# Kernel optimization log

Measured on AMD Instinct MI355X. Metric: run time of the kernel, lower is better.

Reference implementation:

```python
import jax, jax.numpy as jnp
import numpy as np

HEADS = 64
VOCAB = 5
EPS = 1e-5

def _layer_norm(x, g, b):
    mu = jnp.mean(x, axis=-1, keepdims=True)
    var = jnp.var(x, axis=-1, keepdims=True)
    return (x - mu) * jax.lax.rsqrt(var + EPS) * g + b

def setup_inputs() -> dict:
    key = jax.random.key(0)
    ks = jax.random.split(key, 12)
    h = HEADS
    s = 1.0 / np.sqrt(h)
    return {
        "x": jax.random.normal(ks[0], (8, 384, 384, h), dtype=jnp.float32),
        "W1": jax.random.normal(ks[1], (h, h), dtype=jnp.float32) * s,
        "b1": jnp.zeros((h,), jnp.float32),
        "W2": jax.random.normal(ks[2], (h, h), dtype=jnp.float32) * s,
        "b2": jnp.zeros((h,), jnp.float32),
        "W3": jax.random.normal(ks[3], (h, h), dtype=jnp.float32) * s,
        "b3": jnp.zeros((h,), jnp.float32),
        "ln_g": jnp.ones((h,), jnp.float32),
        "ln_b": jnp.zeros((h,), jnp.float32),
        "Wo": jax.random.normal(ks[4], (h, VOCAB), dtype=jnp.float32) * s,
        "bo": jnp.zeros((VOCAB,), jnp.float32),
    }

def reference(x, W1, b1, W2, b2, W3, b3, ln_g, ln_b, Wo, bo):
    # three (Linear -> gelu -> shared LayerNorm) blocks on [b,s,s,h]
    h = _layer_norm(jax.nn.gelu(x @ W1 + b1, approximate=False), ln_g, ln_b)
    h = _layer_norm(jax.nn.gelu(h @ W2 + b2, approximate=False), ln_g, ln_b)
    h = _layer_norm(jax.nn.gelu(h @ W3 + b3, approximate=False), ln_g, ln_b)
    out = h @ Wo + bo  # [b,s,s,vocab]
    return (out + jnp.swapaxes(out, 1, 2)) * 0.5
```

## Files before the change

kernel.cpp:

```cpp
#include <hip/hip_runtime.h>
#include <cstdint>
#include <cstddef>

typedef __attribute__((ext_vector_type(8))) __bf16   bf16x8;
typedef __attribute__((ext_vector_type(2))) __bf16   bf16x2;
typedef __attribute__((ext_vector_type(4))) float    f32x4;
typedef __attribute__((ext_vector_type(4))) uint32_t u32x4;

#define N_ROWS   1179648
#define N_TILES  73728
#define BLOCKS   2048
#define TPW      9
#define SDIM     384
#define VOCAB    5

#define WO_OFF   24576
#define BIAS_OFF 26624
#define OUT_OFF  27392

__device__ __forceinline__ f32x4 gelu4(f32x4 x){
  f32x4 u = x * x;
  f32x4 w = u * (-0.10294456f) + (-2.3021255f);
  f32x4 z = x * w;
  f32x4 e;
  e[0] = __builtin_amdgcn_exp2f(z[0]);
  e[1] = __builtin_amdgcn_exp2f(z[1]);
  e[2] = __builtin_amdgcn_exp2f(z[2]);
  e[3] = __builtin_amdgcn_exp2f(z[3]);
  f32x4 d = e + 1.0f;
  f32x4 r;
  r[0] = __builtin_amdgcn_rcpf(d[0]);
  r[1] = __builtin_amdgcn_rcpf(d[1]);
  r[2] = __builtin_amdgcn_rcpf(d[2]);
  r[3] = __builtin_amdgcn_rcpf(d[3]);
  return x * r;
}

__device__ __forceinline__ bf16x8 mk_bf8(f32x4 a, f32x4 b){
  bf16x8 v;
  v[0]=(__bf16)a[0]; v[1]=(__bf16)a[1]; v[2]=(__bf16)a[2]; v[3]=(__bf16)a[3];
  v[4]=(__bf16)b[0]; v[5]=(__bf16)b[1]; v[6]=(__bf16)b[2]; v[7]=(__bf16)b[3];
  return v;
}

__device__ __forceinline__ int perm_rho(int m){
  return (m & 0x23) | ((m & 4) << 2) | ((m & 0x18) >> 1);
}

__global__ __launch_bounds__(256, 4)
void mlp_kernel(const float* __restrict__ x,
                const float* __restrict__ W1, const float* __restrict__ b1,
                const float* __restrict__ W2, const float* __restrict__ b2,
                const float* __restrict__ W3, const float* __restrict__ b3,
                const float* __restrict__ lng, const float* __restrict__ lnb,
                const float* __restrict__ Wo,  const float* __restrict__ bo,
                float* __restrict__ tmp)
{
  __shared__ __align__(16) uint8_t Wl[28672];

  const int tid = threadIdx.x;

  {
    int m = tid & 63, g = tid >> 6;
    int rho = perm_rho(m);
    uint8_t* wrow = Wl + rho * 128;
    int swz = (rho & 7) << 4;
    #pragma unroll 1
    for (int idx = g; idx < 96; idx += 4) {
      int L = idx >> 5, kp = idx & 31;
      const float* W = (L == 0) ? W1 : ((L == 1) ? W2 : W3);
      float g0 = (L == 0) ? 1.0f : lng[2 * kp];
      float g1 = (L == 0) ? 1.0f : lng[2 * kp + 1];
      float lo = W[(2 * kp    ) * 64 + m] * g0;
      float hi = W[(2 * kp + 1) * 64 + m] * g1;
      bf16x2 p = { (__bf16)lo, (__bf16)hi };
      *(uint32_t*)(wrow + L * 8192 + ((4 * kp) ^ swz)) = __builtin_bit_cast(uint32_t, p);
    }
    int mm = tid & 15;
    #pragma unroll 1
    for (int kp = tid >> 4; kp < 32; kp += 16) {
      float g0 = lng[2 * kp], g1 = lng[2 * kp + 1];
      float lo = (mm < VOCAB) ? Wo[(2 * kp    ) * VOCAB + mm] * g0 : 0.0f;
      float hi = (mm < VOCAB) ? Wo[(2 * kp + 1) * VOCAB + mm] * g1 : 0.0f;
      bf16x2 p = { (__bf16)lo, (__bf16)hi };
      *(uint32_t*)(Wl + WO_OFF + mm * 128 + ((4 * kp) ^ ((mm & 7) << 4))) =
          __builtin_bit_cast(uint32_t, p);
    }
    if (tid < 128) {
      int m2 = tid & 63;
      const float* W = (tid < 64) ? W2 : W3;
      float d = (tid < 64) ? b2[m2] : b3[m2];
      #pragma unroll 4
      for (int k = 0; k < 64; ++k) d = __builtin_fmaf(W[k * 64 + m2], lnb[k], d);
      *(float*)(Wl + BIAS_OFF + (64 + tid) * 4) = d;
    } else if (tid < 192) {
      *(float*)(Wl + BIAS_OFF + (tid - 128) * 4) = b1[tid - 128];
    }
  }
  __syncthreads();

  const int wav  = tid >> 6, lane = tid & 63;
  const int h    = lane >> 4;
  const int b    = lane & 15;
  const int swzW = (b & 7) << 4;
  const int rowB = b * 128;
  const int kOff = 16 * h;
  const float* biasL = (const float*)(Wl + BIAS_OFF);
  float* myF = (float*)(Wl + OUT_OFF) + wav * 80;

  f32x4 aoInit;
  #pragma unroll
  for (int r = 0; r < 4; ++r) {
    int v = 4 * h + r;
    aoInit[r] = (v < VOCAB) ? bo[v] : 0.0f;
  }
  #pragma unroll 4
  for (int k = 0; k < 64; ++k) {
    float l = lnb[k];
    #pragma unroll
    for (int r = 0; r < 4; ++r) {
      int v = 4 * h + r;
      if (v < VOCAB) aoInit[r] = __builtin_fmaf(l, Wo[k * VOCAB + v], aoInit[r]);
    }
  }

  const int gw = blockIdx.x * 4 + wav;
  int t = gw * TPW;

  f32x4 xn[4];
  {
    const float* px = x + (size_t)(t * 16 + b) * 64 + 8 * h;
    xn[0] = *(const f32x4*)(px);      xn[1] = *(const f32x4*)(px + 4);
    xn[2] = *(const f32x4*)(px + 32); xn[3] = *(const f32x4*)(px + 36);
  }

  #pragma unroll 1
  for (int i = 0; i < TPW; ++i, ++t) {
    u32x4 bfr[2];
    bfr[0] = __builtin_bit_cast(u32x4, mk_bf8(xn[0], xn[1]));
    bfr[1] = __builtin_bit_cast(u32x4, mk_bf8(xn[2], xn[3]));

    {
      int tn = (i + 1 < TPW) ? (t + 1) : t;
      const float* pn = x + (size_t)(tn * 16 + b) * 64 + 8 * h;
      xn[0] = *(const f32x4*)(pn);      xn[1] = *(const f32x4*)(pn + 4);
      xn[2] = *(const f32x4*)(pn + 32); xn[3] = *(const f32x4*)(pn + 36);
    }

    #pragma unroll
    for (int L = 0; L < 3; ++L) {
      const uint8_t* wp = Wl + L * 8192 + rowB;
      f32x4 acc[4];
      #pragma unroll
      for (int mt = 0; mt < 4; ++mt) {
        u32x4 w0 = *(const u32x4*)(wp + mt * 2048 + ((kOff     ) ^ swzW));
        u32x4 w1 = *(const u32x4*)(wp + mt * 2048 + ((kOff + 64) ^ swzW));
        int base = 8 * h + 4 * (mt & 1) + 32 * (mt >> 1);
        acc[mt] = *(const f32x4*)(biasL + L * 64 + base);
        acc[mt] = __builtin_amdgcn_mfma_f32_16x16x32_bf16(
            __builtin_bit_cast(bf16x8, w0), __builtin_bit_cast(bf16x8, bfr[0]), acc[mt], 0, 0, 0);
        acc[mt] = __builtin_amdgcn_mfma_f32_16x16x32_bf16(
            __builtin_bit_cast(bf16x8, w1), __builtin_bit_cast(bf16x8, bfr[1]), acc[mt], 0, 0, 0);
      }

      #pragma unroll
      for (int mt = 0; mt < 4; ++mt) acc[mt] = gelu4(acc[mt]);

      f32x4 vs = acc[0] + acc[1] + acc[2] + acc[3];
      f32x4 vq = acc[0]*acc[0] + acc[1]*acc[1] + acc[2]*acc[2] + acc[3]*acc[3];
      float s1 = (vs[0]+vs[1]) + (vs[2]+vs[3]);
      float s2 = (vq[0]+vq[1]) + (vq[2]+vq[3]);
      s1 += __shfl_xor(s1, 16); s2 += __shfl_xor(s2, 16);
      s1 += __shfl_xor(s1, 32); s2 += __shfl_xor(s2, 32);
      float mu   = s1 * (1.0f/64.0f);
      float var  = __builtin_fmaf(s2, (1.0f/64.0f), -mu * mu);
      float rstd = rsqrtf(var + 1e-5f);
      float nm   = -mu * rstd;

      f32x4 n0 = acc[0] * rstd + nm;
      f32x4 n1 = acc[1] * rstd + nm;
      f32x4 n2 = acc[2] * rstd + nm;
      f32x4 n3 = acc[3] * rstd + nm;
      bfr[0] = __builtin_bit_cast(u32x4, mk_bf8(n0, n1));
      bfr[1] = __builtin_bit_cast(u32x4, mk_bf8(n2, n3));
    }

    f32x4 ao = aoInit;
    {
      const uint8_t* wp = Wl + WO_OFF + rowB;
      u32x4 w0 = *(const u32x4*)(wp + ((kOff     ) ^ swzW));
      u32x4 w1 = *(const u32x4*)(wp + ((kOff + 64) ^ swzW));
      ao = __builtin_amdgcn_mfma_f32_16x16x32_bf16(
          __builtin_bit_cast(bf16x8, w0), __builtin_bit_cast(bf16x8, bfr[0]), ao, 0, 0, 0);
      ao = __builtin_amdgcn_mfma_f32_16x16x32_bf16(
          __builtin_bit_cast(bf16x8, w1), __builtin_bit_cast(bf16x8, bfr[1]), ao, 0, 0, 0);
    }

    #pragma unroll
    for (int r = 0; r < 4; ++r) {
      int v = 4 * h + r;
      if (v < VOCAB) myF[b * VOCAB + v] = ao[r];
    }
    float* dst = tmp + (size_t)t * 80;
    dst[lane] = myF[lane];
    if (lane < 16) dst[64 + lane] = myF[64 + lane];
  }
}

__global__ __launch_bounds__(256)
void sym_kernel(const float* __restrict__ tmp, float* __restrict__ out)
{
  __shared__ float A[32][164];
  __shared__ float B[32][164];
  int bid = blockIdx.x;
  int bb = bid / 144, r2 = bid - bb * 144;
  int ti = r2 / 12,  tj = r2 - ti * 12;
  int i0 = ti * 32,  j0 = tj * 32;
  const size_t base = (size_t)bb * SDIM * SDIM;

  for (int idx = threadIdx.x; idx < 32 * 160; idx += 256) {
    int r = idx / 160, c = idx - r * 160;
    A[r][c] = tmp[(base + (size_t)(i0 + r) * SDIM + j0) * VOCAB + c];
    B[r][c] = tmp[(base + (size_t)(j0 + r) * SDIM + i0) * VOCAB + c];
  }
  __syncthreads();
  for (int idx = threadIdx.x; idx < 32 * 160; idx += 256) {
    int r = idx / 160, c = idx - r * 160;
    int jc = c / 5, v = c - jc * 5;
    out[(base + (size_t)(i0 + r) * SDIM + j0) * VOCAB + c] =
        0.5f * (A[r][c] + B[jc][r * 5 + v]);
  }
}

extern "C" void kernel_launch(void* const* d_in, const int* in_sizes, int n_in,
                              void* d_out, int out_size, void* d_ws, size_t ws_size,
                              hipStream_t stream)
{
  const float* x   = (const float*)d_in[0];
  const float* W1  = (const float*)d_in[1];
  const float* b1  = (const float*)d_in[2];
  const float* W2  = (const float*)d_in[3];
  const float* b2  = (const float*)d_in[4];
  const float* W3  = (const float*)d_in[5];
  const float* b3  = (const float*)d_in[6];
  const float* lng = (const float*)d_in[7];
  const float* lnb = (const float*)d_in[8];
  const float* Wo  = (const float*)d_in[9];
  const float* bo  = (const float*)d_in[10];

  float* tmp = (float*)d_ws;
  float* out = (float*)d_out;

  mlp_kernel<<<BLOCKS, 256, 0, stream>>>(x, W1, b1, W2, b2, W3, b3,
                                         lng, lnb, Wo, bo, tmp);
  sym_kernel<<<8 * 12 * 12, 256, 0, stream>>>(tmp, out);
}
```

Baseline: 167.8 us.

## Fold LayerNorm normalization into following matmul epilogue via precomputed weight sums

Instead of normalizing the activations before each bf16 pack, the kernel packs the raw gelu outputs and applies rstd and the mean correction after the next MFMA. It uses precomputed per-column sums of gamma-scaled weights, stored in extra LDS. This removes the per-element normalize step before packing and moves the work to the accumulator epilogue. It also drops the occupancy hint from launch bounds. Numerics change because unnormalized values are rounded to bf16, which risks precision loss for large-magnitude activations.

```diff
diff --git a/kernel.cpp b/kernel.cpp
--- a/kernel.cpp
+++ b/kernel.cpp
@@ -16,7 +16,7 @@
 
 #define WO_OFF   24576
 #define BIAS_OFF 26624
-#define OUT_OFF  27392
+#define OUT_OFF  27904
 
 __device__ __forceinline__ f32x4 gelu4(f32x4 x){
   f32x4 u = x * x;
@@ -47,7 +47,7 @@
   return (m & 0x23) | ((m & 4) << 2) | ((m & 0x18) >> 1);
 }
 
-__global__ __launch_bounds__(256, 4)
+__global__ __launch_bounds__(256)
 void mlp_kernel(const float* __restrict__ x,
                 const float* __restrict__ W1, const float* __restrict__ b1,
                 const float* __restrict__ W2, const float* __restrict__ b2,
@@ -56,7 +56,7 @@
                 const float* __restrict__ Wo,  const float* __restrict__ bo,
                 float* __restrict__ tmp)
 {
-  __shared__ __align__(16) uint8_t Wl[28672];
+  __shared__ __align__(16) uint8_t Wl[29184];
 
   const int tid = threadIdx.x;
 
@@ -90,9 +90,15 @@
       int m2 = tid & 63;
       const float* W = (tid < 64) ? W2 : W3;
       float d = (tid < 64) ? b2[m2] : b3[m2];
+      float s = 0.0f;
       #pragma unroll 4
-      for (int k = 0; k < 64; ++k) d = __builtin_fmaf(W[k * 64 + m2], lnb[k], d);
-      *(float*)(Wl + BIAS_OFF + (64 + tid) * 4) = d;
+      for (int k = 0; k < 64; ++k) {
+        float w = W[k * 64 + m2];
+        d = __builtin_fmaf(w, lnb[k], d);
+        s = __builtin_fmaf(w, lng[k], s);
+      }
+      *(float*)(Wl + BIAS_OFF + (64  + tid) * 4) = d;
+      *(float*)(Wl + BIAS_OFF + (192 + tid) * 4) = s;
     } else if (tid < 192) {
       *(float*)(Wl + BIAS_OFF + (tid - 128) * 4) = b1[tid - 128];
     }
@@ -108,19 +114,24 @@
   const float* biasL = (const float*)(Wl + BIAS_OFF);
   float* myF = (float*)(Wl + OUT_OFF) + wav * 80;
 
-  f32x4 aoInit;
+  f32x4 aoInit, wsoInit;
   #pragma unroll
   for (int r = 0; r < 4; ++r) {
     int v = 4 * h + r;
-    aoInit[r] = (v < VOCAB) ? bo[v] : 0.0f;
+    aoInit[r]  = (v < VOCAB) ? bo[v] : 0.0f;
+    wsoInit[r] = 0.0f;
   }
   #pragma unroll 4
   for (int k = 0; k < 64; ++k) {
-    float l = lnb[k];
+    float lb = lnb[k], lg = lng[k];
     #pragma unroll
     for (int r = 0; r < 4; ++r) {
       int v = 4 * h + r;
-      if (v < VOCAB) aoInit[r] = __builtin_fmaf(l, Wo[k * VOCAB + v], aoInit[r]);
+      if (v < VOCAB) {
+        float w = Wo[k * VOCAB + v];
+        aoInit[r]  = __builtin_fmaf(lb, w, aoInit[r]);
+        wsoInit[r] = __builtin_fmaf(lg, w, wsoInit[r]);
+      }
     }
   }
 
@@ -134,6 +145,8 @@
     xn[2] = *(const f32x4*)(px + 32); xn[3] = *(const f32x4*)(px + 36);
   }
 
+  const f32x4 zf = { 0.0f, 0.0f, 0.0f, 0.0f };
+
   #pragma unroll 1
   for (int i = 0; i < TPW; ++i, ++t) {
     u32x4 bfr[2];
@@ -147,22 +160,22 @@
       xn[2] = *(const f32x4*)(pn + 32); xn[3] = *(const f32x4*)(pn + 36);
     }
 
-    #pragma unroll
-    for (int L = 0; L < 3; ++L) {
-      const uint8_t* wp = Wl + L * 8192 + rowB;
+    float rstd, nm;
+
+    {
+      const uint8_t* wp = Wl + rowB;
       f32x4 acc[4];
       #pragma unroll
       for (int mt = 0; mt < 4; ++mt) {
         u32x4 w0 = *(const u32x4*)(wp + mt * 2048 + ((kOff     ) ^ swzW));
         u32x4 w1 = *(const u32x4*)(wp + mt * 2048 + ((kOff + 64) ^ swzW));
         int base = 8 * h + 4 * (mt & 1) + 32 * (mt >> 1);
-        acc[mt] = *(const f32x4*)(biasL + L * 64 + base);
+        acc[mt] = *(const f32x4*)(biasL + base);
         acc[mt] = __builtin_amdgcn_mfma_f32_16x16x32_bf16(
             __builtin_bit_cast(bf16x8, w0), __builtin_bit_cast(bf16x8, bfr[0]), acc[mt], 0, 0, 0);
         acc[mt] = __builtin_amdgcn_mfma_f32_16x16x32_bf16(
             __builtin_bit_cast(bf16x8, w1), __builtin_bit_cast(bf16x8, bfr[1]), acc[mt], 0, 0, 0);
       }
-
       #pragma unroll
       for (int mt = 0; mt < 4; ++mt) acc[mt] = gelu4(acc[mt]);
 
@@ -172,28 +185,63 @@
       float s2 = (vq[0]+vq[1]) + (vq[2]+vq[3]);
       s1 += __shfl_xor(s1, 16); s2 += __shfl_xor(s2, 16);
       s1 += __shfl_xor(s1, 32); s2 += __shfl_xor(s2, 32);
-      float mu   = s1 * (1.0f/64.0f);
-      float var  = __builtin_fmaf(s2, (1.0f/64.0f), -mu * mu);
-      float rstd = rsqrtf(var + 1e-5f);
-      float nm   = -mu * rstd;
-
-      f32x4 n0 = acc[0] * rstd + nm;
-      f32x4 n1 = acc[1] * rstd + nm;
-      f32x4 n2 = acc[2] * rstd + nm;
-      f32x4 n3 = acc[3] * rstd + nm;
-      bfr[0] = __builtin_bit_cast(u32x4, mk_bf8(n0, n1));
-      bfr[1] = __builtin_bit_cast(u32x4, mk_bf8(n2, n3));
-    }
-
-    f32x4 ao = aoInit;
+      float mu  = s1 * (1.0f/64.0f);
+      float var = __builtin_fmaf(s2, (1.0f/64.0f), -mu * mu);
+      rstd = rsqrtf(var + 1e-5f);
+      nm   = -mu * rstd;
+      bfr[0] = __builtin_bit_cast(u32x4, mk_bf8(acc[0], acc[1]));
+      bfr[1] = __builtin_bit_cast(u32x4, mk_bf8(acc[2], acc[3]));
+    }
+
+    #pragma unroll
+    for (int L = 1; L < 3; ++L) {
+      const uint8_t* wp = Wl + L * 8192 + rowB;
+      f32x4 acc[4];
+      #pragma unroll
+      for (int mt = 0; mt < 4; ++mt) {
+        u32x4 w0 = *(const u32x4*)(wp + mt * 2048 + ((kOff     ) ^ swzW));
+        u32x4 w1 = *(const u32x4*)(wp + mt * 2048 + ((kOff + 64) ^ swzW));
+        acc[mt] = __builtin_amdgcn_mfma_f32_16x16x32_bf16(
+            __builtin_bit_cast(bf16x8, w0), __builtin_bit_cast(bf16x8, bfr[0]), zf, 0, 0, 0);
+        acc[mt] = __builtin_amdgcn_mfma_f32_16x16x32_bf16(
+            __builtin_bit_cast(bf16x8, w1), __builtin_bit_cast(bf16x8, bfr[1]), acc[mt], 0, 0, 0);
+      }
+      #pragma unroll
+      for (int mt = 0; mt < 4; ++mt) {
+        int base = 8 * h + 4 * (mt & 1) + 32 * (mt >> 1);
+        f32x4 bb = *(const f32x4*)(biasL + (L    ) * 64 + base);
+        f32x4 ws = *(const f32x4*)(biasL + (L+2) * 64 + base);
+        f32x4 tv = ws * nm + bb;
+        acc[mt] = acc[mt] * rstd + tv;
+      }
+      #pragma unroll
+      for (int mt = 0; mt < 4; ++mt) acc[mt] = gelu4(acc[mt]);
+
+      f32x4 vs = acc[0] + acc[1] + acc[2] + acc[3];
+      f32x4 vq = acc[0]*acc[0] + acc[1]*acc[1] + acc[2]*acc[2] + acc[3]*acc[3];
+      float s1 = (vs[0]+vs[1]) + (vs[2]+vs[3]);
+      float s2 = (vq[0]+vq[1]) + (vq[2]+vq[3]);
+      s1 += __shfl_xor(s1, 16); s2 += __shfl_xor(s2, 16);
+      s1 += __shfl_xor(s1, 32); s2 += __shfl_xor(s2, 32);
+      float mu  = s1 * (1.0f/64.0f);
+      float var = __builtin_fmaf(s2, (1.0f/64.0f), -mu * mu);
+      rstd = rsqrtf(var + 1e-5f);
+      nm   = -mu * rstd;
+      bfr[0] = __builtin_bit_cast(u32x4, mk_bf8(acc[0], acc[1]));
+      bfr[1] = __builtin_bit_cast(u32x4, mk_bf8(acc[2], acc[3]));
+    }
+
+    f32x4 ao;
     {
       const uint8_t* wp = Wl + WO_OFF + rowB;
       u32x4 w0 = *(const u32x4*)(wp + ((kOff     ) ^ swzW));
       u32x4 w1 = *(const u32x4*)(wp + ((kOff + 64) ^ swzW));
       ao = __builtin_amdgcn_mfma_f32_16x16x32_bf16(
-          __builtin_bit_cast(bf16x8, w0), __builtin_bit_cast(bf16x8, bfr[0]), ao, 0, 0, 0);
+          __builtin_bit_cast(bf16x8, w0), __builtin_bit_cast(bf16x8, bfr[0]), zf, 0, 0, 0);
       ao = __builtin_amdgcn_mfma_f32_16x16x32_bf16(
           __builtin_bit_cast(bf16x8, w1), __builtin_bit_cast(bf16x8, bfr[1]), ao, 0, 0, 0);
+      f32x4 tv = wsoInit * nm + aoInit;
+      ao = ao * rstd + tv;
     }
 
     #pragma unroll
```

Measured after the change: 183.1 us. 9.1% more time.
